# Kernel tuning notes

Measured on AMD Instinct MI355X. Metric: run time of the kernel, lower is better.

The kernel has to match this reference:

```python
import jax, jax.numpy as jnp
import numpy as np

B, S, D, H, HID = 8192, 16, 128, 8, 1024
DH = D // H  # 16
GCN, NUMF = 40, 103
EPS = 1e-5

def _make_pe():
    pos = np.arange(S, dtype=np.float64)[:, None]
    i = np.arange(D, dtype=np.float64)[None, :]
    pe = pos / np.power(10000.0, (i // 2 * 2.0) / D)
    pe[:, 0::2] = np.sin(pe[:, 0::2])
    pe[:, 1::2] = np.cos(pe[:, 1::2])
    return jnp.asarray(pe, dtype=jnp.float32)  # [S, D]

PE = _make_pe()

def setup_inputs() -> dict:
    key = jax.random.key(0)
    ks = jax.random.split(key, 16)
    rn = lambda k, shape, s=0.02: (jax.random.normal(k, shape, jnp.float32) * s)
    return {
        "x": jax.random.normal(ks[0], (B, S, D), jnp.float32),
        "gcn_i": jax.random.normal(ks[1], (B, GCN), jnp.float32),
        "num": jax.random.normal(ks[2], (B, NUMF), jnp.float32),
        # two independent encoder layers, params stacked on leading dim
        "Wq": rn(ks[3], (2, D, D)), "bq": jnp.zeros((2, D), jnp.float32),
        "Wk": rn(ks[4], (2, D, D)), "bk": jnp.zeros((2, D), jnp.float32),
        "Wv": rn(ks[5], (2, D, D)), "bv": jnp.zeros((2, D), jnp.float32),
        "Wo": rn(ks[6], (2, D, D)), "bo": jnp.zeros((2, D), jnp.float32),
        "ln1_g": jnp.ones((2, D), jnp.float32), "ln1_b": jnp.zeros((2, D), jnp.float32),
        "W1": rn(ks[7], (2, D, HID)), "b1": jnp.zeros((2, HID), jnp.float32),
        "W2": rn(ks[8], (2, HID, D)), "b2": jnp.zeros((2, D), jnp.float32),
        "ln2_g": jnp.ones((2, D), jnp.float32), "ln2_b": jnp.zeros((2, D), jnp.float32),
        # head
        "Wn": rn(ks[9], (NUMF, D)), "bnum": jnp.zeros((D,), jnp.float32),
        "bn_gamma": jnp.ones((D,), jnp.float32), "bn_beta": jnp.zeros((D,), jnp.float32),
        "Wf": rn(ks[10], (S * D + GCN + D, 1)), "bf": jnp.zeros((1,), jnp.float32),
    }

def _ln(x, g, b):
    m = x.mean(-1, keepdims=True)
    v = ((x - m) ** 2).mean(-1, keepdims=True)
    return (x - m) * jax.lax.rsqrt(v + EPS) * g + b

def reference(x, gcn_i, num, Wq, bq, Wk, bk, Wv, bv, Wo, bo, ln1_g, ln1_b,
              W1, b1, W2, b2, ln2_g, ln2_b, Wn, bnum, bn_gamma, bn_beta, Wf, bf):
    out = x + PE  # positional encoding (dropout = identity in eval)
    scale = DH ** -0.5
    for l in range(2):
        # NOTE: original uses a raw .view(B*H, -1, DH) (no transpose) -- faithful reshape
        q = (out @ Wq[l] + bq[l]).reshape(B * H, S, DH)
        k = (out @ Wk[l] + bk[l]).reshape(B * H, S, DH)
        v = (out @ Wv[l] + bv[l]).reshape(B * H, S, DH)
        attn = jax.nn.softmax(jnp.einsum('nsd,ntd->nst', q, k) * scale, axis=-1)
        ctx = jnp.einsum('nst,ntd->nsd', attn, v).reshape(B, S, D)
        h = _ln(ctx @ Wo[l] + bo[l] + out, ln1_g[l], ln1_b[l])
        ff = jax.nn.relu(h @ W1[l] + b1[l]) @ W2[l] + b2[l]
        out = _ln(ff + h, ln2_g[l], ln2_b[l])
    flat = out.reshape(B, S * D)  # [B, 2048]
    n = num @ Wn + bnum  # [B, 128]
    # BatchNorm1d, training-mode forward (biased batch variance)
    mu = n.mean(0)
    var = ((n - mu) ** 2).mean(0)
    n = (n - mu) * jax.lax.rsqrt(var + EPS) * bn_gamma + bn_beta
    p = jnp.concatenate([flat, gcn_i, n], axis=-1)  # [B, 2216]
    return jax.nn.sigmoid(p @ Wf + bf)
```

## Files before the change

kernel.cpp:

```cpp
#include <hip/hip_runtime.h>
#include <hip/hip_bf16.h>
#include <math.h>

#define B_SZ   8192
#define S_SZ   16
#define D_SZ   128
#define HID_SZ 1024
#define NUMF_SZ 103
#define GCN_SZ 40
#define G_B    4
#define NBLK   (B_SZ / G_B)
#define SBLK   512
#define STRD   136

typedef short bh8 __attribute__((ext_vector_type(8)));
typedef float fx4 __attribute__((ext_vector_type(4)));
typedef unsigned short us4 __attribute__((ext_vector_type(4)));

__device__ __forceinline__ fx4 mfma16(bh8 a, bh8 b, fx4 c) {
    return __builtin_amdgcn_mfma_f32_16x16x32_bf16(a, b, c, 0, 0, 0);
}

__device__ __forceinline__ unsigned short f2b(float f) {
    union { __hip_bfloat16 b; unsigned short u; } cv;
    cv.b = __float2bfloat16(f);
    return cv.u;
}
__device__ __forceinline__ float bu2f(unsigned short u) {
    return __uint_as_float(((unsigned)u) << 16);
}

__global__ __launch_bounds__(256) void prep_weights(
    const float* __restrict__ Wq, const float* __restrict__ Wk,
    const float* __restrict__ Wv, const float* __restrict__ Wo,
    const float* __restrict__ W1, const float* __restrict__ W2,
    unsigned short* __restrict__ WswQ, unsigned short* __restrict__ WswK,
    unsigned short* __restrict__ WswV, unsigned short* __restrict__ WswO,
    unsigned short* __restrict__ Wsw1, unsigned short* __restrict__ Wsw2,
    float* __restrict__ PEt)
{
    int j = blockIdx.x * 256 + threadIdx.x;
    if (j < 2048) {
        int s = j >> 7, c = j & 127;
        float expo = (float)((c >> 1) * 2) * (1.0f / 128.0f);
        float denom = powf(10000.0f, expo);
        float ang = (float)s / denom;
        PEt[j] = (c & 1) ? cosf(ang) : sinf(ang);
    }
    if (j < 2 * 16384) {
        int r = j & 16383, l = j >> 14;
        int k = r >> 7, n = r & 127;
        int dst = (((l * 8 + (n >> 4)) * 4 + (k >> 5)) * 64 +
                   (((k >> 3) & 3) * 16 + (n & 15))) * 8 + (k & 7);
        WswQ[dst] = f2b(Wq[j]); WswK[dst] = f2b(Wk[j]);
        WswV[dst] = f2b(Wv[j]); WswO[dst] = f2b(Wo[j]);
    }
    {
        int l = j >> 17, r = j & 131071;
        int k = r >> 10, n = r & 1023;
        int dst = (((l * 64 + (n >> 4)) * 4 + (k >> 5)) * 64 +
                   (((k >> 3) & 3) * 16 + (n & 15))) * 8 + (k & 7);
        Wsw1[dst] = f2b(W1[j]);
    }
    {
        int l = j >> 17, r = j & 131071;
        int k = r >> 7, n = r & 127;
        int dst = (((l * 8 + (n >> 4)) * 32 + (k >> 5)) * 64 +
                   (((k >> 3) & 3) * 16 + (n & 15))) * 8 + (k & 7);
        Wsw2[dst] = f2b(W2[j]);
    }
}

__global__ __launch_bounds__(256, 2) void encoder_fused(
    const float* __restrict__ x, const float* __restrict__ gcn,
    const float* __restrict__ bq, const float* __restrict__ bk,
    const float* __restrict__ bv, const float* __restrict__ bo,
    const float* __restrict__ ln1g, const float* __restrict__ ln1b,
    const float* __restrict__ b1, const float* __restrict__ b2p,
    const float* __restrict__ ln2g, const float* __restrict__ ln2b,
    const float* __restrict__ Wf,
    const unsigned short* __restrict__ WswQ, const unsigned short* __restrict__ WswK,
    const unsigned short* __restrict__ WswV, const unsigned short* __restrict__ WswO,
    const unsigned short* __restrict__ Wsw1, const unsigned short* __restrict__ Wsw2,
    const float* __restrict__ PEt,
    const float* __restrict__ num, const float* __restrict__ Wn,
    const float* __restrict__ bnum,
    float* __restrict__ ssum, float* __restrict__ ssq,
    unsigned int* __restrict__ cnt,
    const float* __restrict__ bng, const float* __restrict__ bnb,
    const float* __restrict__ bfin, float* __restrict__ cvec,
    float* __restrict__ acc1)
{
    __shared__ unsigned short ACT[64][STRD];
    __shared__ unsigned short Qb[64][STRD];
    __shared__ unsigned short Kb[64][STRD];
    __shared__ unsigned short Vb[64][STRD];
    __shared__ float2 LNp2[64][4];
    __shared__ unsigned short Pb[4][16][16];
    __shared__ int lastf;

    unsigned short* Vb4 = &Vb[0][0];

    const int t = threadIdx.x;
    const int w = t >> 6, lane = t & 63;
    const int q = lane >> 4, ln = lane & 15;

    if (blockIdx.x >= NBLK) {
        float* NUMs = (float*)ACT;
        float* cred = (float*)Qb;
        float* cS   = (float*)Vb;
        float* redw = (float*)LNp2;
        const int b0 = (blockIdx.x - NBLK) * 16;
        const int j = t & 127, sg = t >> 7, s0 = sg * 8;

        for (int idx = t; idx < 16 * NUMF_SZ; idx += 256) {
            int r = idx / NUMF_SZ, f = idx - r * NUMF_SZ;
            NUMs[r * 104 + f] = num[(size_t)(b0 + r) * NUMF_SZ + f];
        }
        __syncthreads();

        float acc[8];
        float bnv = bnum[j];
#pragma unroll
        for (int r = 0; r < 8; ++r) acc[r] = bnv;
        for (int f = 0; f < NUMF_SZ; ++f) {
            float wv = Wn[f * 128 + j];
#pragma unroll
            for (int r = 0; r < 8; ++r) acc[r] = fmaf(NUMs[(s0 + r) * 104 + f], wv, acc[r]);
        }
        float lsum = 0.f, lsq = 0.f;
#pragma unroll
        for (int r = 0; r < 8; ++r) {
            lsum += acc[r];
            lsq = fmaf(acc[r], acc[r], lsq);
        }
        cred[sg * 128 + j] = lsum;
        cred[(2 + sg) * 128 + j] = lsq;
        __syncthreads();
        if (sg == 0) atomicAdd(&ssum[j], cred[j] + cred[128 + j]);
        else         atomicAdd(&ssq[j],  cred[256 + j] + cred[384 + j]);
        __syncthreads();
        if (t == 0) lastf = (atomicAdd(cnt, 1u) == SBLK - 1u) ? 1 : 0;
        __syncthreads();

        if (lastf) {
            float C1p = 0.f;
            if (t < 128) {
                float sv = atomicAdd(&ssum[t], 0.f);
                float qv = atomicAdd(&ssq[t], 0.f);
                float mean = sv * (1.0f / (float)B_SZ);
                float var = qv * (1.0f / (float)B_SZ) - mean * mean;
                float inv = rsqrtf(var + 1e-5f);
                float wj = Wf[2088 + t];
                float gi = bng[t] * inv;
                float cj = gi * wj;
                cS[t] = cj;
                C1p = (bnb[t] - mean * gi) * wj + bnum[t] * cj;
            }
#pragma unroll
            for (int o = 32; o; o >>= 1) C1p += __shfl_xor(C1p, o);
            if (lane == 0) redw[w] = C1p;
            __syncthreads();
            if (t == 0) cvec[103] = redw[0] + redw[1] + redw[2] + redw[3] + bfin[0];
            if (t < NUMF_SZ) {
                float s2 = 0.f;
                for (int jj = 0; jj < 128; ++jj)
                    s2 = fmaf(Wn[t * 128 + jj], cS[jj], s2);
                cvec[t] = s2;
            }
        }
        return;
    }

    const int bbase = blockIdx.x * G_B;

    {
        const float4* xb = (const float4*)(x + (size_t)bbase * 2048);
        const float4* pe4 = (const float4*)PEt;
#pragma unroll
        for (int i = 0; i < 8; ++i) {
            int f4 = i * 256 + t;
            float4 xv = xb[f4];
            float4 pv = pe4[f4 & 511];
            int flat = f4 * 4;
            int row = flat >> 7, col = flat & 127;
            ushort4 pk = {f2b(xv.x + pv.x), f2b(xv.y + pv.y),
                          f2b(xv.z + pv.z), f2b(xv.w + pv.w)};
            *(ushort4*)&ACT[row][col] = pk;
        }
    }
    __syncthreads();

    for (int l = 0; l < 2; ++l) {
        {
            bh8 afr[4][4];
#pragma unroll
            for (int mt = 0; mt < 4; ++mt)
#pragma unroll
                for (int ks = 0; ks < 4; ++ks)
                    afr[mt][ks] = *(const bh8*)&ACT[mt * 16 + ln][ks * 32 + q * 8];
#pragma unroll
            for (int mtx = 0; mtx < 2; ++mtx) {
                const unsigned short* Wm = (mtx == 0) ? WswQ + l * 16384 : WswK + l * 16384;
                const float* bias = (mtx == 0) ? bq + l * 128 : bk + l * 128;
                unsigned short (*dst)[STRD] = (mtx == 0) ? Qb : Kb;
#pragma unroll
                for (int i2 = 0; i2 < 2; ++i2) {
                    int nt = w * 2 + i2;
                    bh8 wfr[4];
#pragma unroll
                    for (int ks = 0; ks < 4; ++ks)
                        wfr[ks] = *(const bh8*)(Wm + ((nt * 4 + ks) * 64 + lane) * 8);
                    int n0 = nt * 16 + q * 4;
                    fx4 bb4 = *(const fx4*)&bias[n0];
#pragma unroll
                    for (int mt = 0; mt < 4; ++mt) {
                        fx4 acc = {0.f, 0.f, 0.f, 0.f};
#pragma unroll
                        for (int ks = 0; ks < 4; ++ks) acc = mfma16(wfr[ks], afr[mt][ks], acc);
                        us4 o;
#pragma unroll
                        for (int r2 = 0; r2 < 4; ++r2) o[r2] = f2b(acc[r2] + bb4[r2]);
                        *(us4*)&dst[mt * 16 + ln][n0] = o;
                    }
                }
            }
#pragma unroll
            for (int i2 = 0; i2 < 2; ++i2) {
                int nt = w * 2 + i2;
                bh8 wfr[4];
#pragma unroll
                for (int ks = 0; ks < 4; ++ks)
                    wfr[ks] = *(const bh8*)(WswV + l * 16384 + ((nt * 4 + ks) * 64 + lane) * 8);
                int n = nt * 16 + ln;
                float bb = bv[l * 128 + n];
#pragma unroll
                for (int mt = 0; mt < 4; ++mt) {
                    fx4 acc = {0.f, 0.f, 0.f, 0.f};
#pragma unroll
                    for (int ks = 0; ks < 4; ++ks) acc = mfma16(afr[mt][ks], wfr[ks], acc);
#pragma unroll
                    for (int r2 = 0; r2 < 4; ++r2) {
                        int s = q * 4 + r2;
                        Vb4[(((mt * 8 + (s >> 1)) * 16) + ln) * 16 +
                            (((s & 1) << 3) | nt)] = f2b(acc[r2] + bb);
                    }
                }
            }
        }
        __syncthreads();

        {
            const int E = w;
            const int rbase = E * 16 + (ln >> 3);
            const int ccol = (ln & 7) * 16;
#pragma unroll
            for (int g = 0; g < 8; ++g) {
                bh8 kfr = 0, qfr = 0;
                if (q < 2) {
                    kfr = *(const bh8*)&Kb[rbase + 2 * g][ccol + q * 8];
                    qfr = *(const bh8*)&Qb[rbase + 2 * g][ccol + q * 8];
                }
                fx4 st = mfma16(kfr, qfr, fx4{0.f, 0.f, 0.f, 0.f});
                float p0 = st[0] * 0.25f, p1 = st[1] * 0.25f;
                float p2 = st[2] * 0.25f, p3 = st[3] * 0.25f;
                float mx = fmaxf(fmaxf(p0, p1), fmaxf(p2, p3));
                mx = fmaxf(mx, __shfl_xor(mx, 16));
                mx = fmaxf(mx, __shfl_xor(mx, 32));
                p0 = __expf(p0 - mx); p1 = __expf(p1 - mx);
                p2 = __expf(p2 - mx); p3 = __expf(p3 - mx);
                float sm = (p0 + p1) + (p2 + p3);
                sm += __shfl_xor(sm, 16);
                sm += __shfl_xor(sm, 32);
                float is = 1.0f / sm;
                ushort4 pk = {f2b(p0 * is), f2b(p1 * is), f2b(p2 * is), f2b(p3 * is)};
                *(ushort4*)&Pb[w][ln][q * 4] = pk;
                bh8 vfr = 0, pfr = 0;
                if (q < 2) {
                    vfr = *(const bh8*)&Vb4[(((E * 8 + g) * 16) + ln) * 16 + q * 8];
                    pfr = *(const bh8*)&Pb[w][ln][q * 8];
                }
                fx4 cx = mfma16(vfr, pfr, fx4{0.f, 0.f, 0.f, 0.f});
                ushort4 ck = {f2b(cx[0]), f2b(cx[1]), f2b(cx[2]), f2b(cx[3])};
                *(ushort4*)&Qb[rbase + 2 * g][ccol + q * 4] = ck;
            }
        }
        __syncthreads();

        fx4 Cv[2][4];
        {
            bh8 cfr[4][4];
#pragma unroll
            for (int mt = 0; mt < 4; ++mt)
#pragma unroll
                for (int ks = 0; ks < 4; ++ks)
                    cfr[mt][ks] = *(const bh8*)&Qb[mt * 16 + ln][ks * 32 + q * 8];
#pragma unroll
            for (int i2 = 0; i2 < 2; ++i2) {
                int nt = w * 2 + i2, n0 = nt * 16 + q * 4;
                bh8 wfr[4];
#pragma unroll
                for (int ks = 0; ks < 4; ++ks)
                    wfr[ks] = *(const bh8*)(WswO + l * 16384 + ((nt * 4 + ks) * 64 + lane) * 8);
                fx4 bb4 = *(const fx4*)&bo[l * 128 + n0];
#pragma unroll
                for (int mt = 0; mt < 4; ++mt) {
                    fx4 acc = {0.f, 0.f, 0.f, 0.f};
#pragma unroll
                    for (int ks = 0; ks < 4; ++ks) acc = mfma16(wfr[ks], cfr[mt][ks], acc);
                    us4 rv = *(const us4*)&ACT[mt * 16 + ln][n0];
#pragma unroll
                    for (int r2 = 0; r2 < 4; ++r2)
                        Cv[i2][mt][r2] = acc[r2] + bb4[r2] + bu2f(rv[r2]);
                }
            }
        }
#pragma unroll
        for (int mt = 0; mt < 4; ++mt) {
            float s = 0.f, v = 0.f;
#pragma unroll
            for (int i2 = 0; i2 < 2; ++i2)
#pragma unroll
                for (int r2 = 0; r2 < 4; ++r2) {
                    float a = Cv[i2][mt][r2];
                    s += a; v = fmaf(a, a, v);
                }
            s += __shfl_xor(s, 16); v += __shfl_xor(v, 16);
            s += __shfl_xor(s, 32); v += __shfl_xor(v, 32);
            if (lane < 16) LNp2[mt * 16 + ln][w] = float2{s, v};
        }
        __syncthreads();
        {
            float mean4[4], inv4[4];
#pragma unroll
            for (int mt = 0; mt < 4; ++mt) {
                int row = mt * 16 + ln;
                float2 a0 = LNp2[row][0], a1 = LNp2[row][1];
                float2 a2 = LNp2[row][2], a3 = LNp2[row][3];
                float s = (a0.x + a1.x) + (a2.x + a3.x);
                float v = (a0.y + a1.y) + (a2.y + a3.y);
                float mean = s * (1.0f / 128.0f);
                mean4[mt] = mean;
                inv4[mt] = rsqrtf(v * (1.0f / 128.0f) - mean * mean + 1e-5f);
            }
#pragma unroll
            for (int i2 = 0; i2 < 2; ++i2) {
                int n0 = (w * 2 + i2) * 16 + q * 4;
                fx4 gg = *(const fx4*)&ln1g[l * 128 + n0];
                fx4 be = *(const fx4*)&ln1b[l * 128 + n0];
#pragma unroll
                for (int mt = 0; mt < 4; ++mt) {
                    us4 o;
#pragma unroll
                    for (int r2 = 0; r2 < 4; ++r2)
                        o[r2] = f2b((Cv[i2][mt][r2] - mean4[mt]) * inv4[mt] * gg[r2] + be[r2]);
                    *(us4*)&Kb[mt * 16 + ln][n0] = o;
                }
            }
        }
        __syncthreads();

        bh8 hfr[4][4];
#pragma unroll
        for (int mt = 0; mt < 4; ++mt)
#pragma unroll
            for (int ks = 0; ks < 4; ++ks)
                hfr[mt][ks] = *(const bh8*)&Kb[mt * 16 + ln][ks * 32 + q * 8];
        fx4 f2a[2][4];
#pragma unroll
        for (int i2 = 0; i2 < 2; ++i2)
#pragma unroll
            for (int mt = 0; mt < 4; ++mt) f2a[i2][mt] = fx4{0.f, 0.f, 0.f, 0.f};
        for (int ch = 0; ch < 8; ++ch) {
            unsigned short (*dst)[STRD] = (ch & 1) ? Vb : Qb;
            bh8 w1fr[2][4];
#pragma unroll
            for (int i2 = 0; i2 < 2; ++i2) {
                int ntg = ch * 8 + w * 2 + i2;
#pragma unroll
                for (int ks = 0; ks < 4; ++ks)
                    w1fr[i2][ks] = *(const bh8*)(Wsw1 + l * 131072 + ((ntg * 4 + ks) * 64 + lane) * 8);
            }
#pragma unroll
            for (int mt = 0; mt < 4; ++mt) {
#pragma unroll
                for (int i2 = 0; i2 < 2; ++i2) {
                    fx4 acc = {0.f, 0.f, 0.f, 0.f};
#pragma unroll
                    for (int ks = 0; ks < 4; ++ks) acc = mfma16(w1fr[i2][ks], hfr[mt][ks], acc);
                    int nl0 = (w * 2 + i2) * 16 + q * 4;
                    fx4 bb4 = *(const fx4*)&b1[l * HID_SZ + ch * 128 + nl0];
                    us4 o;
#pragma unroll
                    for (int r2 = 0; r2 < 4; ++r2) {
                        float vv = acc[r2] + bb4[r2];
                        o[r2] = f2b(vv > 0.f ? vv : 0.f);
                    }
                    *(us4*)&dst[mt * 16 + ln][nl0] = o;
                }
            }
            __syncthreads();
            bh8 w2fr[2][4];
#pragma unroll
            for (int i2 = 0; i2 < 2; ++i2)
#pragma unroll
                for (int ks = 0; ks < 4; ++ks)
                    w2fr[i2][ks] = *(const bh8*)(Wsw2 + l * 131072 +
                        (((w * 2 + i2) * 32 + ch * 4 + ks) * 64 + lane) * 8);
#pragma unroll
            for (int mt = 0; mt < 4; ++mt) {
                bh8 ffr[4];
#pragma unroll
                for (int ks = 0; ks < 4; ++ks)
                    ffr[ks] = *(const bh8*)&dst[mt * 16 + ln][ks * 32 + q * 8];
#pragma unroll
                for (int i2 = 0; i2 < 2; ++i2)
#pragma unroll
                    for (int ks = 0; ks < 4; ++ks)
                        f2a[i2][mt] = mfma16(w2fr[i2][ks], ffr[ks], f2a[i2][mt]);
            }
        }
        fx4 Cv2[2][4];
#pragma unroll
        for (int i2 = 0; i2 < 2; ++i2) {
            int n0 = (w * 2 + i2) * 16 + q * 4;
            fx4 bb4 = *(const fx4*)&b2p[l * 128 + n0];
#pragma unroll
            for (int mt = 0; mt < 4; ++mt) {
                us4 rv = *(const us4*)&Kb[mt * 16 + ln][n0];
#pragma unroll
                for (int r2 = 0; r2 < 4; ++r2)
                    Cv2[i2][mt][r2] = f2a[i2][mt][r2] + bb4[r2] + bu2f(rv[r2]);
            }
        }
#pragma unroll
        for (int mt = 0; mt < 4; ++mt) {
            float s = 0.f, v = 0.f;
#pragma unroll
            for (int i2 = 0; i2 < 2; ++i2)
#pragma unroll
                for (int r2 = 0; r2 < 4; ++r2) {
                    float a = Cv2[i2][mt][r2];
                    s += a; v = fmaf(a, a, v);
                }
            s += __shfl_xor(s, 16); v += __shfl_xor(v, 16);
            s += __shfl_xor(s, 32); v += __shfl_xor(v, 32);
            if (lane < 16) LNp2[mt * 16 + ln][w] = float2{s, v};
        }
        __syncthreads();
        {
            float mean4[4], inv4[4];
#pragma unroll
            for (int mt = 0; mt < 4; ++mt) {
                int row = mt * 16 + ln;
                float2 a0 = LNp2[row][0], a1 = LNp2[row][1];
                float2 a2 = LNp2[row][2], a3 = LNp2[row][3];
                float s = (a0.x + a1.x) + (a2.x + a3.x);
                float v = (a0.y + a1.y) + (a2.y + a3.y);
                float mean = s * (1.0f / 128.0f);
                mean4[mt] = mean;
                inv4[mt] = rsqrtf(v * (1.0f / 128.0f) - mean * mean + 1e-5f);
            }
#pragma unroll
            for (int i2 = 0; i2 < 2; ++i2) {
                int n0 = (w * 2 + i2) * 16 + q * 4;
                fx4 gg = *(const fx4*)&ln2g[l * 128 + n0];
                fx4 be = *(const fx4*)&ln2b[l * 128 + n0];
#pragma unroll
                for (int mt = 0; mt < 4; ++mt) {
                    us4 o;
#pragma unroll
                    for (int r2 = 0; r2 < 4; ++r2)
                        o[r2] = f2b((Cv2[i2][mt][r2] - mean4[mt]) * inv4[mt] * gg[r2] + be[r2]);
                    *(us4*)&ACT[mt * 16 + ln][n0] = o;
                }
            }
        }
        __syncthreads();
    }

    {
        int bg = bbase + w;
        float part = 0.f;
        int srow = lane >> 2, c0 = (lane & 3) * 32;
#pragma unroll
        for (int i = 0; i < 4; ++i) {
            bh8 av = *(const bh8*)&ACT[w * 16 + srow][c0 + i * 8];
            int fl = srow * 128 + c0 + i * 8;
#pragma unroll
            for (int e = 0; e < 8; ++e)
                part = fmaf(bu2f((unsigned short)av[e]), Wf[fl + e], part);
        }
        if (lane < GCN_SZ)
            part = fmaf(gcn[(size_t)bg * GCN_SZ + lane], Wf[2048 + lane], part);
#pragma unroll
        for (int off = 32; off; off >>= 1) part += __shfl_xor(part, off);
        if (lane == 0) acc1[bg] = part;
    }
}

__global__ __launch_bounds__(256) void final_fast(
    const float* __restrict__ num, const float* __restrict__ cvec,
    const float* __restrict__ acc1, float* __restrict__ out)
{
    __shared__ float wv[104];
    const int t = threadIdx.x;
    if (t < 104) wv[t] = cvec[t];
    __syncthreads();
    const int w = t >> 6, lane = t & 63;
    const int b = blockIdx.x * 4 + w;
    const float* nb = num + (size_t)b * NUMF_SZ;
    float part = nb[lane] * wv[lane];
    if (lane < NUMF_SZ - 64) part += nb[64 + lane] * wv[64 + lane];
#pragma unroll
    for (int o = 32; o; o >>= 1) part += __shfl_xor(part, o);
    if (lane == 0)
        out[b] = 1.0f / (1.0f + __expf(-(acc1[b] + part + wv[103])));
}

extern "C" void kernel_launch(void* const* d_in, const int* in_sizes, int n_in,
                              void* d_out, int out_size, void* d_ws, size_t ws_size,
                              hipStream_t stream)
{
    const float* x    = (const float*)d_in[0];
    const float* gcn  = (const float*)d_in[1];
    const float* num  = (const float*)d_in[2];
    const float* Wq   = (const float*)d_in[3];
    const float* bq   = (const float*)d_in[4];
    const float* Wk   = (const float*)d_in[5];
    const float* bk   = (const float*)d_in[6];
    const float* Wv   = (const float*)d_in[7];
    const float* bv   = (const float*)d_in[8];
    const float* Wo   = (const float*)d_in[9];
    const float* bo   = (const float*)d_in[10];
    const float* ln1g = (const float*)d_in[11];
    const float* ln1b = (const float*)d_in[12];
    const float* W1   = (const float*)d_in[13];
    const float* b1   = (const float*)d_in[14];
    const float* W2   = (const float*)d_in[15];
    const float* b2p  = (const float*)d_in[16];
    const float* ln2g = (const float*)d_in[17];
    const float* ln2b = (const float*)d_in[18];
    const float* Wn   = (const float*)d_in[19];
    const float* bnum = (const float*)d_in[20];
    const float* bng  = (const float*)d_in[21];
    const float* bnb  = (const float*)d_in[22];
    const float* Wf   = (const float*)d_in[23];
    const float* bfin = (const float*)d_in[24];

    float* acc1 = (float*)d_ws;
    float* ssum = acc1 + B_SZ;
    float* ssq  = ssum + 128;
    unsigned int* cnt = (unsigned int*)(ssq + 128);
    unsigned short* wb = (unsigned short*)((char*)d_ws + 40960);
    unsigned short* WswQ = wb;
    unsigned short* WswK = wb + 32768;
    unsigned short* WswV = wb + 65536;
    unsigned short* WswO = wb + 98304;
    unsigned short* Wsw1 = wb + 131072;
    unsigned short* Wsw2 = wb + 393216;
    float* PEt = (float*)((char*)d_ws + 40960 + 1310720);
    float* cvec = (float*)((char*)d_ws + 40960 + 1310720 + 8192);

    hipMemsetAsync(ssum, 0, 257 * sizeof(float), stream);
    prep_weights<<<1024, 256, 0, stream>>>(Wq, Wk, Wv, Wo, W1, W2,
        WswQ, WswK, WswV, WswO, Wsw1, Wsw2, PEt);
    encoder_fused<<<NBLK + SBLK, 256, 0, stream>>>(x, gcn, bq, bk, bv, bo,
        ln1g, ln1b, b1, b2p, ln2g, ln2b, Wf,
        WswQ, WswK, WswV, WswO, Wsw1, Wsw2, PEt,
        num, Wn, bnum, ssum, ssq, cnt, bng, bnb, bfin, cvec, acc1);
    final_fast<<<B_SZ / 4, 256, 0, stream>>>(num, cvec, acc1, (float*)d_out);
}
```

Before: 393.9 us.

## Merge prep, encoder and head into one persistent cooperative kernel with grid syncs

Replaces the memset, prep_weights, encoder_fused and final_fast launches with a single cooperative persistent kernel. It uses grid-wide syncs between the weight-conversion phase, the encoder/batch-norm phase and the final output phase, and the grid is sized from occupancy. This aims to remove launch gaps and the atomic last-block counter, at the cost of grid-barrier overhead and a fixed grid of at most 512 blocks looping over the 2048 encoder tiles.

```diff
diff --git a/kernel.cpp b/kernel.cpp
--- a/kernel.cpp
+++ b/kernel.cpp
@@ -1,6 +1,9 @@
 #include <hip/hip_runtime.h>
+#include <hip/hip_cooperative_groups.h>
 #include <hip/hip_bf16.h>
 #include <math.h>
+
+namespace cg = cooperative_groups;
 
 #define B_SZ   8192
 #define S_SZ   16
@@ -20,7 +23,6 @@
 __device__ __forceinline__ fx4 mfma16(bh8 a, bh8 b, fx4 c) {
     return __builtin_amdgcn_mfma_f32_16x16x32_bf16(a, b, c, 0, 0, 0);
 }
-
 __device__ __forceinline__ unsigned short f2b(float f) {
     union { __hip_bfloat16 b; unsigned short u; } cv;
     cv.b = __float2bfloat16(f);
@@ -30,66 +32,20 @@
     return __uint_as_float(((unsigned)u) << 16);
 }
 
-__global__ __launch_bounds__(256) void prep_weights(
-    const float* __restrict__ Wq, const float* __restrict__ Wk,
-    const float* __restrict__ Wv, const float* __restrict__ Wo,
-    const float* __restrict__ W1, const float* __restrict__ W2,
-    unsigned short* __restrict__ WswQ, unsigned short* __restrict__ WswK,
-    unsigned short* __restrict__ WswV, unsigned short* __restrict__ WswO,
-    unsigned short* __restrict__ Wsw1, unsigned short* __restrict__ Wsw2,
-    float* __restrict__ PEt)
-{
-    int j = blockIdx.x * 256 + threadIdx.x;
-    if (j < 2048) {
-        int s = j >> 7, c = j & 127;
-        float expo = (float)((c >> 1) * 2) * (1.0f / 128.0f);
-        float denom = powf(10000.0f, expo);
-        float ang = (float)s / denom;
-        PEt[j] = (c & 1) ? cosf(ang) : sinf(ang);
-    }
-    if (j < 2 * 16384) {
-        int r = j & 16383, l = j >> 14;
-        int k = r >> 7, n = r & 127;
-        int dst = (((l * 8 + (n >> 4)) * 4 + (k >> 5)) * 64 +
-                   (((k >> 3) & 3) * 16 + (n & 15))) * 8 + (k & 7);
-        WswQ[dst] = f2b(Wq[j]); WswK[dst] = f2b(Wk[j]);
-        WswV[dst] = f2b(Wv[j]); WswO[dst] = f2b(Wo[j]);
-    }
-    {
-        int l = j >> 17, r = j & 131071;
-        int k = r >> 10, n = r & 1023;
-        int dst = (((l * 64 + (n >> 4)) * 4 + (k >> 5)) * 64 +
-                   (((k >> 3) & 3) * 16 + (n & 15))) * 8 + (k & 7);
-        Wsw1[dst] = f2b(W1[j]);
-    }
-    {
-        int l = j >> 17, r = j & 131071;
-        int k = r >> 7, n = r & 127;
-        int dst = (((l * 8 + (n >> 4)) * 32 + (k >> 5)) * 64 +
-                   (((k >> 3) & 3) * 16 + (n & 15))) * 8 + (k & 7);
-        Wsw2[dst] = f2b(W2[j]);
-    }
-}
-
-__global__ __launch_bounds__(256, 2) void encoder_fused(
-    const float* __restrict__ x, const float* __restrict__ gcn,
-    const float* __restrict__ bq, const float* __restrict__ bk,
-    const float* __restrict__ bv, const float* __restrict__ bo,
-    const float* __restrict__ ln1g, const float* __restrict__ ln1b,
-    const float* __restrict__ b1, const float* __restrict__ b2p,
-    const float* __restrict__ ln2g, const float* __restrict__ ln2b,
-    const float* __restrict__ Wf,
-    const unsigned short* __restrict__ WswQ, const unsigned short* __restrict__ WswK,
-    const unsigned short* __restrict__ WswV, const unsigned short* __restrict__ WswO,
-    const unsigned short* __restrict__ Wsw1, const unsigned short* __restrict__ Wsw2,
-    const float* __restrict__ PEt,
-    const float* __restrict__ num, const float* __restrict__ Wn,
-    const float* __restrict__ bnum,
-    float* __restrict__ ssum, float* __restrict__ ssq,
-    unsigned int* __restrict__ cnt,
-    const float* __restrict__ bng, const float* __restrict__ bnb,
-    const float* __restrict__ bfin, float* __restrict__ cvec,
-    float* __restrict__ acc1)
+struct KArgs {
+    const float *x, *gcn;
+    const float *bq, *bk, *bv, *bo, *ln1g, *ln1b, *b1, *b2p, *ln2g, *ln2b, *Wf;
+    const float *Wq, *Wk, *Wv, *Wo, *W1, *W2;
+    unsigned short *WswQ, *WswK, *WswV, *WswO, *Wsw1, *Wsw2;
+    float *PEt;
+    const float *num, *Wn, *bnum;
+    float *ssum, *ssq;
+    const float *bng, *bnb, *bfin;
+    float *acc1;
+    float *out;
+};
+
+__global__ __launch_bounds__(256, 2) void mega_coop(KArgs a)
 {
     __shared__ unsigned short ACT[64][STRD];
     __shared__ unsigned short Qb[64][STRD];
@@ -97,7 +53,6 @@
     __shared__ unsigned short Vb[64][STRD];
     __shared__ float2 LNp2[64][4];
     __shared__ unsigned short Pb[4][16][16];
-    __shared__ int lastf;
 
     unsigned short* Vb4 = &Vb[0][0];
 
@@ -105,26 +60,388 @@
     const int w = t >> 6, lane = t & 63;
     const int q = lane >> 4, ln = lane & 15;
 
-    if (blockIdx.x >= NBLK) {
+    for (int j = blockIdx.x * 256 + t; j < 262144; j += gridDim.x * 256) {
+        if (j < 2048) {
+            int s = j >> 7, c = j & 127;
+            float expo = (float)((c >> 1) * 2) * (1.0f / 128.0f);
+            float denom = powf(10000.0f, expo);
+            float ang = (float)s / denom;
+            a.PEt[j] = (c & 1) ? cosf(ang) : sinf(ang);
+        }
+        if (j < 2 * 16384) {
+            int r = j & 16383, l = j >> 14;
+            int k = r >> 7, n = r & 127;
+            int dst = (((l * 8 + (n >> 4)) * 4 + (k >> 5)) * 64 +
+                       (((k >> 3) & 3) * 16 + (n & 15))) * 8 + (k & 7);
+            a.WswQ[dst] = f2b(a.Wq[j]); a.WswK[dst] = f2b(a.Wk[j]);
+            a.WswV[dst] = f2b(a.Wv[j]); a.WswO[dst] = f2b(a.Wo[j]);
+        }
+        {
+            int l = j >> 17, r = j & 131071;
+            int k = r >> 10, n = r & 1023;
+            int dst = (((l * 64 + (n >> 4)) * 4 + (k >> 5)) * 64 +
+                       (((k >> 3) & 3) * 16 + (n & 15))) * 8 + (k & 7);
+            a.Wsw1[dst] = f2b(a.W1[j]);
+        }
+        {
+            int l = j >> 17, r = j & 131071;
+            int k = r >> 7, n = r & 127;
+            int dst = (((l * 8 + (n >> 4)) * 32 + (k >> 5)) * 64 +
+                       (((k >> 3) & 3) * 16 + (n & 15))) * 8 + (k & 7);
+            a.Wsw2[dst] = f2b(a.W2[j]);
+        }
+    }
+    if (blockIdx.x == 0 && t < 256) a.ssum[t] = 0.f;
+    __threadfence();
+    cg::this_grid().sync();
+
+    for (int bt = blockIdx.x; bt < NBLK; bt += gridDim.x) {
+        const int bbase = bt * G_B;
+
+        {
+            const float4* xb = (const float4*)(a.x + (size_t)bbase * 2048);
+            const float4* pe4 = (const float4*)a.PEt;
+#pragma unroll
+            for (int i = 0; i < 8; ++i) {
+                int f4 = i * 256 + t;
+                float4 xv = xb[f4];
+                float4 pv = pe4[f4 & 511];
+                int flat = f4 * 4;
+                int row = flat >> 7, col = flat & 127;
+                ushort4 pk = {f2b(xv.x + pv.x), f2b(xv.y + pv.y),
+                              f2b(xv.z + pv.z), f2b(xv.w + pv.w)};
+                *(ushort4*)&ACT[row][col] = pk;
+            }
+        }
+        __syncthreads();
+
+        for (int l = 0; l < 2; ++l) {
+            {
+                bh8 afr[4][4];
+#pragma unroll
+                for (int mt = 0; mt < 4; ++mt)
+#pragma unroll
+                    for (int ks = 0; ks < 4; ++ks)
+                        afr[mt][ks] = *(const bh8*)&ACT[mt * 16 + ln][ks * 32 + q * 8];
+#pragma unroll
+                for (int mtx = 0; mtx < 2; ++mtx) {
+                    const unsigned short* Wm = (mtx == 0) ? a.WswQ + l * 16384 : a.WswK + l * 16384;
+                    const float* bias = (mtx == 0) ? a.bq + l * 128 : a.bk + l * 128;
+                    unsigned short (*dst)[STRD] = (mtx == 0) ? Qb : Kb;
+#pragma unroll
+                    for (int i2 = 0; i2 < 2; ++i2) {
+                        int nt = w * 2 + i2;
+                        bh8 wfr[4];
+#pragma unroll
+                        for (int ks = 0; ks < 4; ++ks)
+                            wfr[ks] = *(const bh8*)(Wm + ((nt * 4 + ks) * 64 + lane) * 8);
+                        int n0 = nt * 16 + q * 4;
+                        fx4 bb4 = *(const fx4*)&bias[n0];
+#pragma unroll
+                        for (int mt = 0; mt < 4; ++mt) {
+                            fx4 acc = {0.f, 0.f, 0.f, 0.f};
+#pragma unroll
+                            for (int ks = 0; ks < 4; ++ks) acc = mfma16(wfr[ks], afr[mt][ks], acc);
+                            us4 o;
+#pragma unroll
+                            for (int r2 = 0; r2 < 4; ++r2) o[r2] = f2b(acc[r2] + bb4[r2]);
+                            *(us4*)&dst[mt * 16 + ln][n0] = o;
+                        }
+                    }
+                }
+#pragma unroll
+                for (int i2 = 0; i2 < 2; ++i2) {
+                    int nt = w * 2 + i2;
+                    bh8 wfr[4];
+#pragma unroll
+                    for (int ks = 0; ks < 4; ++ks)
+                        wfr[ks] = *(const bh8*)(a.WswV + l * 16384 + ((nt * 4 + ks) * 64 + lane) * 8);
+                    int n = nt * 16 + ln;
+                    float bb = a.bv[l * 128 + n];
+#pragma unroll
+                    for (int mt = 0; mt < 4; ++mt) {
+                        fx4 acc = {0.f, 0.f, 0.f, 0.f};
+#pragma unroll
+                        for (int ks = 0; ks < 4; ++ks) acc = mfma16(afr[mt][ks], wfr[ks], acc);
+#pragma unroll
+                        for (int r2 = 0; r2 < 4; ++r2) {
+                            int s = q * 4 + r2;
+                            Vb4[(((mt * 8 + (s >> 1)) * 16) + ln) * 16 +
+                                (((s & 1) << 3) | nt)] = f2b(acc[r2] + bb);
+                        }
+                    }
+                }
+            }
+            __syncthreads();
+
+            {
+                const int E = w;
+                const int rbase = E * 16 + (ln >> 3);
+                const int ccol = (ln & 7) * 16;
+#pragma unroll
+                for (int g = 0; g < 8; ++g) {
+                    bh8 kfr = 0, qfr = 0;
+                    if (q < 2) {
+                        kfr = *(const bh8*)&Kb[rbase + 2 * g][ccol + q * 8];
+                        qfr = *(const bh8*)&Qb[rbase + 2 * g][ccol + q * 8];
+                    }
+                    fx4 st = mfma16(kfr, qfr, fx4{0.f, 0.f, 0.f, 0.f});
+                    float p0 = st[0] * 0.25f, p1 = st[1] * 0.25f;
+                    float p2 = st[2] * 0.25f, p3 = st[3] * 0.25f;
+                    float mx = fmaxf(fmaxf(p0, p1), fmaxf(p2, p3));
+                    mx = fmaxf(mx, __shfl_xor(mx, 16));
+                    mx = fmaxf(mx, __shfl_xor(mx, 32));
+                    p0 = __expf(p0 - mx); p1 = __expf(p1 - mx);
+                    p2 = __expf(p2 - mx); p3 = __expf(p3 - mx);
+                    float sm = (p0 + p1) + (p2 + p3);
+                    sm += __shfl_xor(sm, 16);
+                    sm += __shfl_xor(sm, 32);
+                    float is = 1.0f / sm;
+                    ushort4 pk = {f2b(p0 * is), f2b(p1 * is), f2b(p2 * is), f2b(p3 * is)};
+                    *(ushort4*)&Pb[w][ln][q * 4] = pk;
+                    bh8 vfr = 0, pfr = 0;
+                    if (q < 2) {
+                        vfr = *(const bh8*)&Vb4[(((E * 8 + g) * 16) + ln) * 16 + q * 8];
+                        pfr = *(const bh8*)&Pb[w][ln][q * 8];
+                    }
+                    fx4 cx = mfma16(vfr, pfr, fx4{0.f, 0.f, 0.f, 0.f});
+                    ushort4 ck = {f2b(cx[0]), f2b(cx[1]), f2b(cx[2]), f2b(cx[3])};
+                    *(ushort4*)&Qb[rbase + 2 * g][ccol + q * 4] = ck;
+                }
+            }
+            __syncthreads();
+
+            fx4 Cv[2][4];
+            {
+                bh8 cfr[4][4];
+#pragma unroll
+                for (int mt = 0; mt < 4; ++mt)
+#pragma unroll
+                    for (int ks = 0; ks < 4; ++ks)
+                        cfr[mt][ks] = *(const bh8*)&Qb[mt * 16 + ln][ks * 32 + q * 8];
+#pragma unroll
+                for (int i2 = 0; i2 < 2; ++i2) {
+                    int nt = w * 2 + i2, n0 = nt * 16 + q * 4;
+                    bh8 wfr[4];
+#pragma unroll
+                    for (int ks = 0; ks < 4; ++ks)
+                        wfr[ks] = *(const bh8*)(a.WswO + l * 16384 + ((nt * 4 + ks) * 64 + lane) * 8);
+                    fx4 bb4 = *(const fx4*)&a.bo[l * 128 + n0];
+#pragma unroll
+                    for (int mt = 0; mt < 4; ++mt) {
+                        fx4 acc = {0.f, 0.f, 0.f, 0.f};
+#pragma unroll
+                        for (int ks = 0; ks < 4; ++ks) acc = mfma16(wfr[ks], cfr[mt][ks], acc);
+                        us4 rv = *(const us4*)&ACT[mt * 16 + ln][n0];
+#pragma unroll
+                        for (int r2 = 0; r2 < 4; ++r2)
+                            Cv[i2][mt][r2] = acc[r2] + bb4[r2] + bu2f(rv[r2]);
+                    }
+                }
+            }
+#pragma unroll
+            for (int mt = 0; mt < 4; ++mt) {
+                float s = 0.f, v = 0.f;
+#pragma unroll
+                for (int i2 = 0; i2 < 2; ++i2)
+#pragma unroll
+                    for (int r2 = 0; r2 < 4; ++r2) {
+                        float aa = Cv[i2][mt][r2];
+                        s += aa; v = fmaf(aa, aa, v);
+                    }
+                s += __shfl_xor(s, 16); v += __shfl_xor(v, 16);
+                s += __shfl_xor(s, 32); v += __shfl_xor(v, 32);
+                if (lane < 16) LNp2[mt * 16 + ln][w] = float2{s, v};
+            }
+            __syncthreads();
+            {
+                float mean4[4], inv4[4];
+#pragma unroll
+                for (int mt = 0; mt < 4; ++mt) {
+                    int row = mt * 16 + ln;
+                    float2 a0 = LNp2[row][0], a1 = LNp2[row][1];
+                    float2 a2 = LNp2[row][2], a3 = LNp2[row][3];
+                    float s = (a0.x + a1.x) + (a2.x + a3.x);
+                    float v = (a0.y + a1.y) + (a2.y + a3.y);
+                    float mean = s * (1.0f / 128.0f);
+                    mean4[mt] = mean;
+                    inv4[mt] = rsqrtf(v * (1.0f / 128.0f) - mean * mean + 1e-5f);
+                }
+#pragma unroll
+                for (int i2 = 0; i2 < 2; ++i2) {
+                    int n0 = (w * 2 + i2) * 16 + q * 4;
+                    fx4 gg = *(const fx4*)&a.ln1g[l * 128 + n0];
+                    fx4 be = *(const fx4*)&a.ln1b[l * 128 + n0];
+#pragma unroll
+                    for (int mt = 0; mt < 4; ++mt) {
+                        us4 o;
+#pragma unroll
+                        for (int r2 = 0; r2 < 4; ++r2)
+                            o[r2] = f2b((Cv[i2][mt][r2] - mean4[mt]) * inv4[mt] * gg[r2] + be[r2]);
+                        *(us4*)&Kb[mt * 16 + ln][n0] = o;
+                    }
+                }
+            }
+            __syncthreads();
+
+            bh8 hfr[4][4];
+#pragma unroll
+            for (int mt = 0; mt < 4; ++mt)
+#pragma unroll
+                for (int ks = 0; ks < 4; ++ks)
+                    hfr[mt][ks] = *(const bh8*)&Kb[mt * 16 + ln][ks * 32 + q * 8];
+            fx4 f2a[2][4];
+#pragma unroll
+            for (int i2 = 0; i2 < 2; ++i2)
+#pragma unroll
+                for (int mt = 0; mt < 4; ++mt) f2a[i2][mt] = fx4{0.f, 0.f, 0.f, 0.f};
+            for (int ch = 0; ch < 8; ++ch) {
+                unsigned short (*dst)[STRD] = (ch & 1) ? Vb : Qb;
+                bh8 w1fr[2][4];
+#pragma unroll
+                for (int i2 = 0; i2 < 2; ++i2) {
+                    int ntg = ch * 8 + w * 2 + i2;
+#pragma unroll
+                    for (int ks = 0; ks < 4; ++ks)
+                        w1fr[i2][ks] = *(const bh8*)(a.Wsw1 + l * 131072 + ((ntg * 4 + ks) * 64 + lane) * 8);
+                }
+#pragma unroll
+                for (int mt = 0; mt < 4; ++mt) {
+#pragma unroll
+                    for (int i2 = 0; i2 < 2; ++i2) {
+                        fx4 acc = {0.f, 0.f, 0.f, 0.f};
+#pragma unroll
+                        for (int ks = 0; ks < 4; ++ks) acc = mfma16(w1fr[i2][ks], hfr[mt][ks], acc);
+                        int nl0 = (w * 2 + i2) * 16 + q * 4;
+                        fx4 bb4 = *(const fx4*)&a.b1[l * HID_SZ + ch * 128 + nl0];
+                        us4 o;
+#pragma unroll
+                        for (int r2 = 0; r2 < 4; ++r2) {
+                            float vv = acc[r2] + bb4[r2];
+                            o[r2] = f2b(vv > 0.f ? vv : 0.f);
+                        }
+                        *(us4*)&dst[mt * 16 + ln][nl0] = o;
+                    }
+                }
+                __syncthreads();
+                bh8 w2fr[2][4];
+#pragma unroll
+                for (int i2 = 0; i2 < 2; ++i2)
+#pragma unroll
+                    for (int ks = 0; ks < 4; ++ks)
+                        w2fr[i2][ks] = *(const bh8*)(a.Wsw2 + l * 131072 +
+                            (((w * 2 + i2) * 32 + ch * 4 + ks) * 64 + lane) * 8);
+#pragma unroll
+                for (int mt = 0; mt < 4; ++mt) {
+                    bh8 ffr[4];
+#pragma unroll
+                    for (int ks = 0; ks < 4; ++ks)
+                        ffr[ks] = *(const bh8*)&dst[mt * 16 + ln][ks * 32 + q * 8];
+#pragma unroll
+                    for (int i2 = 0; i2 < 2; ++i2)
+#pragma unroll
+                        for (int ks = 0; ks < 4; ++ks)
+                            f2a[i2][mt] = mfma16(w2fr[i2][ks], ffr[ks], f2a[i2][mt]);
+                }
+            }
+            fx4 Cv2[2][4];
+#pragma unroll
+            for (int i2 = 0; i2 < 2; ++i2) {
+                int n0 = (w * 2 + i2) * 16 + q * 4;
+                fx4 bb4 = *(const fx4*)&a.b2p[l * 128 + n0];
+#pragma unroll
+                for (int mt = 0; mt < 4; ++mt) {
+                    us4 rv = *(const us4*)&Kb[mt * 16 + ln][n0];
+#pragma unroll
+                    for (int r2 = 0; r2 < 4; ++r2)
+                        Cv2[i2][mt][r2] = f2a[i2][mt][r2] + bb4[r2] + bu2f(rv[r2]);
+                }
+            }
+#pragma unroll
+            for (int mt = 0; mt < 4; ++mt) {
+                float s = 0.f, v = 0.f;
+#pragma unroll
+                for (int i2 = 0; i2 < 2; ++i2)
+#pragma unroll
+                    for (int r2 = 0; r2 < 4; ++r2) {
+                        float aa = Cv2[i2][mt][r2];
+                        s += aa; v = fmaf(aa, aa, v);
+                    }
+                s += __shfl_xor(s, 16); v += __shfl_xor(v, 16);
+                s += __shfl_xor(s, 32); v += __shfl_xor(v, 32);
+                if (lane < 16) LNp2[mt * 16 + ln][w] = float2{s, v};
+            }
+            __syncthreads();
+            {
+                float mean4[4], inv4[4];
+#pragma unroll
+                for (int mt = 0; mt < 4; ++mt) {
+                    int row = mt * 16 + ln;
+                    float2 a0 = LNp2[row][0], a1 = LNp2[row][1];
+                    float2 a2 = LNp2[row][2], a3 = LNp2[row][3];
+                    float s = (a0.x + a1.x) + (a2.x + a3.x);
+                    float v = (a0.y + a1.y) + (a2.y + a3.y);
+                    float mean = s * (1.0f / 128.0f);
+                    mean4[mt] = mean;
+                    inv4[mt] = rsqrtf(v * (1.0f / 128.0f) - mean * mean + 1e-5f);
+                }
+#pragma unroll
+                for (int i2 = 0; i2 < 2; ++i2) {
+                    int n0 = (w * 2 + i2) * 16 + q * 4;
+                    fx4 gg = *(const fx4*)&a.ln2g[l * 128 + n0];
+                    fx4 be = *(const fx4*)&a.ln2b[l * 128 + n0];
+#pragma unroll
+                    for (int mt = 0; mt < 4; ++mt) {
+                        us4 o;
+#pragma unroll
+                        for (int r2 = 0; r2 < 4; ++r2)
+                            o[r2] = f2b((Cv2[i2][mt][r2] - mean4[mt]) * inv4[mt] * gg[r2] + be[r2]);
+                        *(us4*)&ACT[mt * 16 + ln][n0] = o;
+                    }
+                }
+            }
+            __syncthreads();
+        }
+
+        {
+            int bg = bbase + w;
+            float part = 0.f;
+            int srow = lane >> 2, c0 = (lane & 3) * 32;
+#pragma unroll
+            for (int i = 0; i < 4; ++i) {
+                bh8 av = *(const bh8*)&ACT[w * 16 + srow][c0 + i * 8];
+                int fl = srow * 128 + c0 + i * 8;
+#pragma unroll
+                for (int e = 0; e < 8; ++e)
+                    part = fmaf(bu2f((unsigned short)av[e]), a.Wf[fl + e], part);
+            }
+            if (lane < GCN_SZ)
+                part = fmaf(a.gcn[(size_t)bg * GCN_SZ + lane], a.Wf[2048 + lane], part);
+#pragma unroll
+            for (int off = 32; off; off >>= 1) part += __shfl_xor(part, off);
+            if (lane == 0) a.acc1[bg] = part;
+        }
+        __syncthreads();
+    }
+
+    for (int st = blockIdx.x; st < SBLK; st += gridDim.x) {
         float* NUMs = (float*)ACT;
         float* cred = (float*)Qb;
-        float* cS   = (float*)Vb;
-        float* redw = (float*)LNp2;
-        const int b0 = (blockIdx.x - NBLK) * 16;
+        const int b0 = st * 16;
         const int j = t & 127, sg = t >> 7, s0 = sg * 8;
 
         for (int idx = t; idx < 16 * NUMF_SZ; idx += 256) {
             int r = idx / NUMF_SZ, f = idx - r * NUMF_SZ;
-            NUMs[r * 104 + f] = num[(size_t)(b0 + r) * NUMF_SZ + f];
+            NUMs[r * 104 + f] = a.num[(size_t)(b0 + r) * NUMF_SZ + f];
         }
         __syncthreads();
 
         float acc[8];
-        float bnv = bnum[j];
+        float bnv = a.bnum[j];
 #pragma unroll
         for (int r = 0; r < 8; ++r) acc[r] = bnv;
         for (int f = 0; f < NUMF_SZ; ++f) {
-            float wv = Wn[f * 128 + j];
+            float wv = a.Wn[f * 128 + j];
 #pragma unroll
             for (int r = 0; r < 8; ++r) acc[r] = fmaf(NUMs[(s0 + r) * 104 + f], wv, acc[r]);
         }
@@ -137,437 +454,123 @@
         cred[sg * 128 + j] = lsum;
         cred[(2 + sg) * 128 + j] = lsq;
         __syncthreads();
-        if (sg == 0) atomicAdd(&ssum[j], cred[j] + cred[128 + j]);
-        else         atomicAdd(&ssq[j],  cred[256 + j] + cred[384 + j]);
-        __syncthreads();
-        if (t == 0) lastf = (atomicAdd(cnt, 1u) == SBLK - 1u) ? 1 : 0;
-        __syncthreads();
-
-        if (lastf) {
-            float C1p = 0.f;
-            if (t < 128) {
-                float sv = atomicAdd(&ssum[t], 0.f);
-                float qv = atomicAdd(&ssq[t], 0.f);
-                float mean = sv * (1.0f / (float)B_SZ);
-                float var = qv * (1.0f / (float)B_SZ) - mean * mean;
-                float inv = rsqrtf(var + 1e-5f);
-                float wj = Wf[2088 + t];
-                float gi = bng[t] * inv;
-                float cj = gi * wj;
-                cS[t] = cj;
-                C1p = (bnb[t] - mean * gi) * wj + bnum[t] * cj;
-            }
-#pragma unroll
-            for (int o = 32; o; o >>= 1) C1p += __shfl_xor(C1p, o);
-            if (lane == 0) redw[w] = C1p;
-            __syncthreads();
-            if (t == 0) cvec[103] = redw[0] + redw[1] + redw[2] + redw[3] + bfin[0];
-            if (t < NUMF_SZ) {
-                float s2 = 0.f;
-                for (int jj = 0; jj < 128; ++jj)
-                    s2 = fmaf(Wn[t * 128 + jj], cS[jj], s2);
-                cvec[t] = s2;
-            }
-        }
-        return;
+        if (sg == 0) atomicAdd(&a.ssum[j], cred[j] + cred[128 + j]);
+        else         atomicAdd(&a.ssq[j],  cred[256 + j] + cred[384 + j]);
+        __syncthreads();
     }
-
-    const int bbase = blockIdx.x * G_B;
+    __threadfence();
+    cg::this_grid().sync();
 
     {
-        const float4* xb = (const float4*)(x + (size_t)bbase * 2048);
-        const float4* pe4 = (const float4*)PEt;
-#pragma unroll
-        for (int i = 0; i < 8; ++i) {
-            int f4 = i * 256 + t;
-            float4 xv = xb[f4];
-            float4 pv = pe4[f4 & 511];
-            int flat = f4 * 4;
-            int row = flat >> 7, col = flat & 127;
-            ushort4 pk = {f2b(xv.x + pv.x), f2b(xv.y + pv.y),
-                          f2b(xv.z + pv.z), f2b(xv.w + pv.w)};
-            *(ushort4*)&ACT[row][col] = pk;
+        float* cS   = (float*)&Vb[0][0];
+        float* wv   = (float*)&Pb[0][0][0];
+        float* redw = (float*)&LNp2[0][0];
+
+        float C1p = 0.f;
+        if (t < 128) {
+            float sv = atomicAdd(&a.ssum[t], 0.f);
+            float qv = atomicAdd(&a.ssq[t], 0.f);
+            float mean = sv * (1.0f / (float)B_SZ);
+            float var = qv * (1.0f / (float)B_SZ) - mean * mean;
+            float inv = rsqrtf(var + 1e-5f);
+            float wj = a.Wf[2088 + t];
+            float gi = a.bng[t] * inv;
+            float cj = gi * wj;
+            cS[t] = cj;
+            C1p = (a.bnb[t] - mean * gi) * wj + a.bnum[t] * cj;
+        }
+#pragma unroll
+        for (int o = 32; o; o >>= 1) C1p += __shfl_xor(C1p, o);
+        if (lane == 0) redw[w] = C1p;
+        __syncthreads();
+        const float C1 = redw[0] + redw[1] + redw[2] + redw[3] + a.bfin[0];
+        if (t < NUMF_SZ) {
+            float s2 = 0.f;
+            for (int jj = 0; jj < 128; ++jj)
+                s2 = fmaf(a.Wn[t * 128 + jj], cS[jj], s2);
+            wv[t] = s2;
+        }
+        __syncthreads();
+
+        for (int st = blockIdx.x; st < SBLK; st += gridDim.x) {
+#pragma unroll
+            for (int rr = 0; rr < 4; ++rr) {
+                int b = st * 16 + w * 4 + rr;
+                const float* nb = a.num + (size_t)b * NUMF_SZ;
+                float part = nb[lane] * wv[lane];
+                if (lane < NUMF_SZ - 64) part += nb[64 + lane] * wv[64 + lane];
+#pragma unroll
+                for (int o = 32; o; o >>= 1) part += __shfl_xor(part, o);
+                if (lane == 0) {
+                    float av = atomicAdd(&a.acc1[b], 0.f);
+                    a.out[b] = 1.0f / (1.0f + __expf(-(av + part + C1)));
+                }
+            }
         }
     }
-    __syncthreads();
-
-    for (int l = 0; l < 2; ++l) {
-        {
-            bh8 afr[4][4];
-#pragma unroll
-            for (int mt = 0; mt < 4; ++mt)
-#pragma unroll
-                for (int ks = 0; ks < 4; ++ks)
-                    afr[mt][ks] = *(const bh8*)&ACT[mt * 16 + ln][ks * 32 + q * 8];
-#pragma unroll
-            for (int mtx = 0; mtx < 2; ++mtx) {
-                const unsigned short* Wm = (mtx == 0) ? WswQ + l * 16384 : WswK + l * 16384;
-                const float* bias = (mtx == 0) ? bq + l * 128 : bk + l * 128;
-                unsigned short (*dst)[STRD] = (mtx == 0) ? Qb : Kb;
-#pragma unroll
-                for (int i2 = 0; i2 < 2; ++i2) {
-                    int nt = w * 2 + i2;
-                    bh8 wfr[4];
-#pragma unroll
-                    for (int ks = 0; ks < 4; ++ks)
-                        wfr[ks] = *(const bh8*)(Wm + ((nt * 4 + ks) * 64 + lane) * 8);
-                    int n0 = nt * 16 + q * 4;
-                    fx4 bb4 = *(const fx4*)&bias[n0];
-#pragma unroll
-                    for (int mt = 0; mt < 4; ++mt) {
-                        fx4 acc = {0.f, 0.f, 0.f, 0.f};
-#pragma unroll
-                        for (int ks = 0; ks < 4; ++ks) acc = mfma16(wfr[ks], afr[mt][ks], acc);
-                        us4 o;
-#pragma unroll
-                        for (int r2 = 0; r2 < 4; ++r2) o[r2] = f2b(acc[r2] + bb4[r2]);
-                        *(us4*)&dst[mt * 16 + ln][n0] = o;
-                    }
-                }
-            }
-#pragma unroll
-            for (int i2 = 0; i2 < 2; ++i2) {
-                int nt = w * 2 + i2;
-                bh8 wfr[4];
-#pragma unroll
-                for (int ks = 0; ks < 4; ++ks)
-                    wfr[ks] = *(const bh8*)(WswV + l * 16384 + ((nt * 4 + ks) * 64 + lane) * 8);
-                int n = nt * 16 + ln;
-                float bb = bv[l * 128 + n];
-#pragma unroll
-                for (int mt = 0; mt < 4; ++mt) {
-                    fx4 acc = {0.f, 0.f, 0.f, 0.f};
-#pragma unroll
-                    for (int ks = 0; ks < 4; ++ks) acc = mfma16(afr[mt][ks], wfr[ks], acc);
-#pragma unroll
-                    for (int r2 = 0; r2 < 4; ++r2) {
-                        int s = q * 4 + r2;
-                        Vb4[(((mt * 8 + (s >> 1)) * 16) + ln) * 16 +
-                            (((s & 1) << 3) | nt)] = f2b(acc[r2] + bb);
-                    }
-                }
-            }
-        }
-        __syncthreads();
-
-        {
-            const int E = w;
-            const int rbase = E * 16 + (ln >> 3);
-            const int ccol = (ln & 7) * 16;
-#pragma unroll
-            for (int g = 0; g < 8; ++g) {
-                bh8 kfr = 0, qfr = 0;
-                if (q < 2) {
-                    kfr = *(const bh8*)&Kb[rbase + 2 * g][ccol + q * 8];
-                    qfr = *(const bh8*)&Qb[rbase + 2 * g][ccol + q * 8];
-                }
-                fx4 st = mfma16(kfr, qfr, fx4{0.f, 0.f, 0.f, 0.f});
-                float p0 = st[0] * 0.25f, p1 = st[1] * 0.25f;
-                float p2 = st[2] * 0.25f, p3 = st[3] * 0.25f;
-                float mx = fmaxf(fmaxf(p0, p1), fmaxf(p2, p3));
-                mx = fmaxf(mx, __shfl_xor(mx, 16));
-                mx = fmaxf(mx, __shfl_xor(mx, 32));
-                p0 = __expf(p0 - mx); p1 = __expf(p1 - mx);
-                p2 = __expf(p2 - mx); p3 = __expf(p3 - mx);
-                float sm = (p0 + p1) + (p2 + p3);
-                sm += __shfl_xor(sm, 16);
-                sm += __shfl_xor(sm, 32);
-                float is = 1.0f / sm;
-                ushort4 pk = {f2b(p0 * is), f2b(p1 * is), f2b(p2 * is), f2b(p3 * is)};
-                *(ushort4*)&Pb[w][ln][q * 4] = pk;
-                bh8 vfr = 0, pfr = 0;
-                if (q < 2) {
-                    vfr = *(const bh8*)&Vb4[(((E * 8 + g) * 16) + ln) * 16 + q * 8];
-                    pfr = *(const bh8*)&Pb[w][ln][q * 8];
-                }
-                fx4 cx = mfma16(vfr, pfr, fx4{0.f, 0.f, 0.f, 0.f});
-                ushort4 ck = {f2b(cx[0]), f2b(cx[1]), f2b(cx[2]), f2b(cx[3])};
-                *(ushort4*)&Qb[rbase + 2 * g][ccol + q * 4] = ck;
-            }
-        }
-        __syncthreads();
-
-        fx4 Cv[2][4];
-        {
-            bh8 cfr[4][4];
-#pragma unroll
-            for (int mt = 0; mt < 4; ++mt)
-#pragma unroll
-                for (int ks = 0; ks < 4; ++ks)
-                    cfr[mt][ks] = *(const bh8*)&Qb[mt * 16 + ln][ks * 32 + q * 8];
-#pragma unroll
-            for (int i2 = 0; i2 < 2; ++i2) {
-                int nt = w * 2 + i2, n0 = nt * 16 + q * 4;
-                bh8 wfr[4];
-#pragma unroll
-                for (int ks = 0; ks < 4; ++ks)
-                    wfr[ks] = *(const bh8*)(WswO + l * 16384 + ((nt * 4 + ks) * 64 + lane) * 8);
-                fx4 bb4 = *(const fx4*)&bo[l * 128 + n0];
-#pragma unroll
-                for (int mt = 0; mt < 4; ++mt) {
-                    fx4 acc = {0.f, 0.f, 0.f, 0.f};
-#pragma unroll
-                    for (int ks = 0; ks < 4; ++ks) acc = mfma16(wfr[ks], cfr[mt][ks], acc);
-                    us4 rv = *(const us4*)&ACT[mt * 16 + ln][n0];
-#pragma unroll
-                    for (int r2 = 0; r2 < 4; ++r2)
-                        Cv[i2][mt][r2] = acc[r2] + bb4[r2] + bu2f(rv[r2]);
-                }
-            }
-        }
-#pragma unroll
-        for (int mt = 0; mt < 4; ++mt) {
-            float s = 0.f, v = 0.f;
-#pragma unroll
-            for (int i2 = 0; i2 < 2; ++i2)
-#pragma unroll
-                for (int r2 = 0; r2 < 4; ++r2) {
-                    float a = Cv[i2][mt][r2];
-                    s += a; v = fmaf(a, a, v);
-                }
-            s += __shfl_xor(s, 16); v += __shfl_xor(v, 16);
-            s += __shfl_xor(s, 32); v += __shfl_xor(v, 32);
-            if (lane < 16) LNp2[mt * 16 + ln][w] = float2{s, v};
-        }
-        __syncthreads();
-        {
-            float mean4[4], inv4[4];
-#pragma unroll
-            for (int mt = 0; mt < 4; ++mt) {
-                int row = mt * 16 + ln;
-                float2 a0 = LNp2[row][0], a1 = LNp2[row][1];
-                float2 a2 = LNp2[row][2], a3 = LNp2[row][3];
-                float s = (a0.x + a1.x) + (a2.x + a3.x);
-                float v = (a0.y + a1.y) + (a2.y + a3.y);
-                float mean = s * (1.0f / 128.0f);
-                mean4[mt] = mean;
-                inv4[mt] = rsqrtf(v * (1.0f / 128.0f) - mean * mean + 1e-5f);
-            }
-#pragma unroll
-            for (int i2 = 0; i2 < 2; ++i2) {
-                int n0 = (w * 2 + i2) * 16 + q * 4;
-                fx4 gg = *(const fx4*)&ln1g[l * 128 + n0];
-                fx4 be = *(const fx4*)&ln1b[l * 128 + n0];
-#pragma unroll
-                for (int mt = 0; mt < 4; ++mt) {
-                    us4 o;
-#pragma unroll
-                    for (int r2 = 0; r2 < 4; ++r2)
-                        o[r2] = f2b((Cv[i2][mt][r2] - mean4[mt]) * inv4[mt] * gg[r2] + be[r2]);
-                    *(us4*)&Kb[mt * 16 + ln][n0] = o;
-                }
-            }
-        }
-        __syncthreads();
-
-        bh8 hfr[4][4];
-#pragma unroll
-        for (int mt = 0; mt < 4; ++mt)
-#pragma unroll
-            for (int ks = 0; ks < 4; ++ks)
-                hfr[mt][ks] = *(const bh8*)&Kb[mt * 16 + ln][ks * 32 + q * 8];
-        fx4 f2a[2][4];
-#pragma unroll
-        for (int i2 = 0; i2 < 2; ++i2)
-#pragma unroll
-            for (int mt = 0; mt < 4; ++mt) f2a[i2][mt] = fx4{0.f, 0.f, 0.f, 0.f};
-        for (int ch = 0; ch < 8; ++ch) {
-            unsigned short (*dst)[STRD] = (ch & 1) ? Vb : Qb;
-            bh8 w1fr[2][4];
-#pragma unroll
-            for (int i2 = 0; i2 < 2; ++i2) {
-                int ntg = ch * 8 + w * 2 + i2;
-#pragma unroll
-                for (int ks = 0; ks < 4; ++ks)
-                    w1fr[i2][ks] = *(const bh8*)(Wsw1 + l * 131072 + ((ntg * 4 + ks) * 64 + lane) * 8);
-            }
-#pragma unroll
-            for (int mt = 0; mt < 4; ++mt) {
-#pragma unroll
-                for (int i2 = 0; i2 < 2; ++i2) {
-                    fx4 acc = {0.f, 0.f, 0.f, 0.f};
-#pragma unroll
-                    for (int ks = 0; ks < 4; ++ks) acc = mfma16(w1fr[i2][ks], hfr[mt][ks], acc);
-                    int nl0 = (w * 2 + i2) * 16 + q * 4;
-                    fx4 bb4 = *(const fx4*)&b1[l * HID_SZ + ch * 128 + nl0];
-                    us4 o;
-#pragma unroll
-                    for (int r2 = 0; r2 < 4; ++r2) {
-                        float vv = acc[r2] + bb4[r2];
-                        o[r2] = f2b(vv > 0.f ? vv : 0.f);
-                    }
-                    *(us4*)&dst[mt * 16 + ln][nl0] = o;
-                }
-            }
-            __syncthreads();
-            bh8 w2fr[2][4];
-#pragma unroll
-            for (int i2 = 0; i2 < 2; ++i2)
-#pragma unroll
-                for (int ks = 0; ks < 4; ++ks)
-                    w2fr[i2][ks] = *(const bh8*)(Wsw2 + l * 131072 +
-                        (((w * 2 + i2) * 32 + ch * 4 + ks) * 64 + lane) * 8);
-#pragma unroll
-            for (int mt = 0; mt < 4; ++mt) {
-                bh8 ffr[4];
-#pragma unroll
-                for (int ks = 0; ks < 4; ++ks)
-                    ffr[ks] = *(const bh8*)&dst[mt * 16 + ln][ks * 32 + q * 8];
-#pragma unroll
-                for (int i2 = 0; i2 < 2; ++i2)
-#pragma unroll
-                    for (int ks = 0; ks < 4; ++ks)
-                        f2a[i2][mt] = mfma16(w2fr[i2][ks], ffr[ks], f2a[i2][mt]);
-            }
-        }
-        fx4 Cv2[2][4];
-#pragma unroll
-        for (int i2 = 0; i2 < 2; ++i2) {
-            int n0 = (w * 2 + i2) * 16 + q * 4;
-            fx4 bb4 = *(const fx4*)&b2p[l * 128 + n0];
-#pragma unroll
-            for (int mt = 0; mt < 4; ++mt) {
-                us4 rv = *(const us4*)&Kb[mt * 16 + ln][n0];
-#pragma unroll
-                for (int r2 = 0; r2 < 4; ++r2)
-                    Cv2[i2][mt][r2] = f2a[i2][mt][r2] + bb4[r2] + bu2f(rv[r2]);
-            }
-        }
-#pragma unroll
-        for (int mt = 0; mt < 4; ++mt) {
-            float s = 0.f, v = 0.f;
-#pragma unroll
-            for (int i2 = 0; i2 < 2; ++i2)
-#pragma unroll
-                for (int r2 = 0; r2 < 4; ++r2) {
-                    float a = Cv2[i2][mt][r2];
-                    s += a; v = fmaf(a, a, v);
-                }
-            s += __shfl_xor(s, 16); v += __shfl_xor(v, 16);
-            s += __shfl_xor(s, 32); v += __shfl_xor(v, 32);
-            if (lane < 16) LNp2[mt * 16 + ln][w] = float2{s, v};
-        }
-        __syncthreads();
-        {
-            float mean4[4], inv4[4];
-#pragma unroll
-            for (int mt = 0; mt < 4; ++mt) {
-                int row = mt * 16 + ln;
-                float2 a0 = LNp2[row][0], a1 = LNp2[row][1];
-                float2 a2 = LNp2[row][2], a3 = LNp2[row][3];
-                float s = (a0.x + a1.x) + (a2.x + a3.x);
-                float v = (a0.y + a1.y) + (a2.y + a3.y);
-                float mean = s * (1.0f / 128.0f);
-                mean4[mt] = mean;
-                inv4[mt] = rsqrtf(v * (1.0f / 128.0f) - mean * mean + 1e-5f);
-            }
-#pragma unroll
-            for (int i2 = 0; i2 < 2; ++i2) {
-                int n0 = (w * 2 + i2) * 16 + q * 4;
-                fx4 gg = *(const fx4*)&ln2g[l * 128 + n0];
-                fx4 be = *(const fx4*)&ln2b[l * 128 + n0];
-#pragma unroll
-                for (int mt = 0; mt < 4; ++mt) {
-                    us4 o;
-#pragma unroll
-                    for (int r2 = 0; r2 < 4; ++r2)
-                        o[r2] = f2b((Cv2[i2][mt][r2] - mean4[mt]) * inv4[mt] * gg[r2] + be[r2]);
-                    *(us4*)&ACT[mt * 16 + ln][n0] = o;
-                }
-            }
-        }
-        __syncthreads();
-    }
-
-    {
-        int bg = bbase + w;
-        float part = 0.f;
-        int srow = lane >> 2, c0 = (lane & 3) * 32;
-#pragma unroll
-        for (int i = 0; i < 4; ++i) {
-            bh8 av = *(const bh8*)&ACT[w * 16 + srow][c0 + i * 8];
-            int fl = srow * 128 + c0 + i * 8;
-#pragma unroll
-            for (int e = 0; e < 8; ++e)
-                part = fmaf(bu2f((unsigned short)av[e]), Wf[fl + e], part);
-        }
-        if (lane < GCN_SZ)
-            part = fmaf(gcn[(size_t)bg * GCN_SZ + lane], Wf[2048 + lane], part);
-#pragma unroll
-        for (int off = 32; off; off >>= 1) part += __shfl_xor(part, off);
-        if (lane == 0) acc1[bg] = part;
-    }
-}
-
-__global__ __launch_bounds__(256) void final_fast(
-    const float* __restrict__ num, const float* __restrict__ cvec,
-    const float* __restrict__ acc1, float* __restrict__ out)
-{
-    __shared__ float wv[104];
-    const int t = threadIdx.x;
-    if (t < 104) wv[t] = cvec[t];
-    __syncthreads();
-    const int w = t >> 6, lane = t & 63;
-    const int b = blockIdx.x * 4 + w;
-    const float* nb = num + (size_t)b * NUMF_SZ;
-    float part = nb[lane] * wv[lane];
-    if (lane < NUMF_SZ - 64) part += nb[64 + lane] * wv[64 + lane];
-#pragma unroll
-    for (int o = 32; o; o >>= 1) part += __shfl_xor(part, o);
-    if (lane == 0)
-        out[b] = 1.0f / (1.0f + __expf(-(acc1[b] + part + wv[103])));
 }
 
 extern "C" void kernel_launch(void* const* d_in, const int* in_sizes, int n_in,
                               void* d_out, int out_size, void* d_ws, size_t ws_size,
                               hipStream_t stream)
 {
-    const float* x    = (const float*)d_in[0];
-    const float* gcn  = (const float*)d_in[1];
-    const float* num  = (const float*)d_in[2];
-    const float* Wq   = (const float*)d_in[3];
-    const float* bq   = (const float*)d_in[4];
-    const float* Wk   = (const float*)d_in[5];
-    const float* bk   = (const float*)d_in[6];
-    const float* Wv   = (const float*)d_in[7];
-    const float* bv   = (const float*)d_in[8];
-    const float* Wo   = (const float*)d_in[9];
-    const float* bo   = (const float*)d_in[10];
-    const float* ln1g = (const float*)d_in[11];
-    const float* ln1b = (const float*)d_in[12];
-    const float* W1   = (const float*)d_in[13];
-    const float* b1   = (const float*)d_in[14];
-    const float* W2   = (const float*)d_in[15];
-    const float* b2p  = (const float*)d_in[16];
-    const float* ln2g = (const float*)d_in[17];
-    const float* ln2b = (const float*)d_in[18];
-    const float* Wn   = (const float*)d_in[19];
-    const float* bnum = (const float*)d_in[20];
-    const float* bng  = (const float*)d_in[21];
-    const float* bnb  = (const float*)d_in[22];
-    const float* Wf   = (const float*)d_in[23];
-    const float* bfin = (const float*)d_in[24];
+    KArgs ka;
+    ka.x    = (const float*)d_in[0];
+    ka.gcn  = (const float*)d_in[1];
+    ka.num  = (const float*)d_in[2];
+    ka.Wq   = (const float*)d_in[3];
+    ka.bq   = (const float*)d_in[4];
+    ka.Wk   = (const float*)d_in[5];
+    ka.bk   = (const float*)d_in[6];
+    ka.Wv   = (const float*)d_in[7];
+    ka.bv   = (const float*)d_in[8];
+    ka.Wo   = (const float*)d_in[9];
+    ka.bo   = (const float*)d_in[10];
+    ka.ln1g = (const float*)d_in[11];
+    ka.ln1b = (const float*)d_in[12];
+    ka.W1   = (const float*)d_in[13];
+    ka.b1   = (const float*)d_in[14];
+    ka.W2   = (const float*)d_in[15];
+    ka.b2p  = (const float*)d_in[16];
+    ka.ln2g = (const float*)d_in[17];
+    ka.ln2b = (const float*)d_in[18];
+    ka.Wn   = (const float*)d_in[19];
+    ka.bnum = (const float*)d_in[20];
+    ka.bng  = (const float*)d_in[21];
+    ka.bnb  = (const float*)d_in[22];
+    ka.Wf   = (const float*)d_in[23];
+    ka.bfin = (const float*)d_in[24];
 
     float* acc1 = (float*)d_ws;
     float* ssum = acc1 + B_SZ;
     float* ssq  = ssum + 128;
-    unsigned int* cnt = (unsigned int*)(ssq + 128);
     unsigned short* wb = (unsigned short*)((char*)d_ws + 40960);
-    unsigned short* WswQ = wb;
-    unsigned short* WswK = wb + 32768;
-    unsigned short* WswV = wb + 65536;
-    unsigned short* WswO = wb + 98304;
-    unsigned short* Wsw1 = wb + 131072;
-    unsigned short* Wsw2 = wb + 393216;
-    float* PEt = (float*)((char*)d_ws + 40960 + 1310720);
-    float* cvec = (float*)((char*)d_ws + 40960 + 1310720 + 8192);
-
-    hipMemsetAsync(ssum, 0, 257 * sizeof(float), stream);
-    prep_weights<<<1024, 256, 0, stream>>>(Wq, Wk, Wv, Wo, W1, W2,
-        WswQ, WswK, WswV, WswO, Wsw1, Wsw2, PEt);
-    encoder_fused<<<NBLK + SBLK, 256, 0, stream>>>(x, gcn, bq, bk, bv, bo,
-        ln1g, ln1b, b1, b2p, ln2g, ln2b, Wf,
-        WswQ, WswK, WswV, WswO, Wsw1, Wsw2, PEt,
-        num, Wn, bnum, ssum, ssq, cnt, bng, bnb, bfin, cvec, acc1);
-    final_fast<<<B_SZ / 4, 256, 0, stream>>>(num, cvec, acc1, (float*)d_out);
+    ka.acc1 = acc1;
+    ka.ssum = ssum;
+    ka.ssq  = ssq;
+    ka.WswQ = wb;
+    ka.WswK = wb + 32768;
+    ka.WswV = wb + 65536;
+    ka.WswO = wb + 98304;
+    ka.Wsw1 = wb + 131072;
+    ka.Wsw2 = wb + 393216;
+    ka.PEt  = (float*)((char*)d_ws + 40960 + 1310720);
+    ka.out  = (float*)d_out;
+
+    static int g_grid = 0;
+    if (g_grid == 0) {
+        int occ = 0;
+        if (hipOccupancyMaxActiveBlocksPerMultiprocessor(&occ, mega_coop, 256, 0)
+                != hipSuccess || occ < 1) occ = 2;
+        int cus = 256;
+        hipDeviceProp_t props;
+        if (hipGetDeviceProperties(&props, 0) == hipSuccess && props.multiProcessorCount > 0)
+            cus = props.multiProcessorCount;
+        g_grid = occ * cus;
+        if (g_grid > 512) g_grid = 512;
+        if (g_grid < 1) g_grid = 256;
+    }
+
+    void* params[] = { (void*)&ka };
+    hipLaunchCooperativeKernel(mega_coop, dim3(g_grid), dim3(256), params, 0u, stream);
 }
```

Measured after the change: 673.1 us. 70.9% more time.
